# Optimization experiments

Measured on AMD Instinct MI355X. Metric: run time of the kernel, lower is better.

The kernel has to match this reference:

```python
import jax, jax.numpy as jnp
import numpy as np

N_NODES = 50000
N_EDGES = 800000
IN_CH, HID_CH, OUT_CH = 100, 128, 47
ORIG_SIZE = 25000


def sage_conv(x, edge_index, w_l, b_l, w_r):
    """PyG-style SAGEConv with mean aggregation.
    out = lin_l(mean_{j in N(i)} x_j) + lin_r(x_i)
    edge_index[0]=source, edge_index[1]=target.
    """
    src, dst = edge_index[0], edge_index[1]
    n = x.shape[0]
    # gather source features, scatter-sum into targets  [N, d]
    agg = jax.ops.segment_sum(x[src], dst, num_segments=n)
    deg = jax.ops.segment_sum(jnp.ones((src.shape[0],), x.dtype), dst, num_segments=n)
    mean = agg / jnp.maximum(deg, 1.0)[:, None]
    return mean @ w_l + b_l + x @ w_r


def setup_inputs() -> dict:
    key = jax.random.key(0)
    ks = jax.random.split(key, 8)
    x = jax.random.normal(ks[0], (N_NODES, IN_CH), dtype=jnp.float32)
    edge_index = jax.random.randint(ks[1], (2, N_EDGES), 0, N_NODES, dtype=jnp.int32)
    s1 = 1.0 / np.sqrt(IN_CH)
    s2 = 1.0 / np.sqrt(HID_CH)
    w1_l = jax.random.uniform(ks[2], (IN_CH, HID_CH), jnp.float32, -s1, s1)
    b1_l = jax.random.uniform(ks[3], (HID_CH,), jnp.float32, -s1, s1)
    w1_r = jax.random.uniform(ks[4], (IN_CH, HID_CH), jnp.float32, -s1, s1)
    w2_l = jax.random.uniform(ks[5], (HID_CH, OUT_CH), jnp.float32, -s2, s2)
    b2_l = jax.random.uniform(ks[6], (OUT_CH,), jnp.float32, -s2, s2)
    w2_r = jax.random.uniform(ks[7], (HID_CH, OUT_CH), jnp.float32, -s2, s2)
    return {"x": x, "edge_index": edge_index, "original_size": ORIG_SIZE,
            "w1_l": w1_l, "b1_l": b1_l, "w1_r": w1_r,
            "w2_l": w2_l, "b2_l": b2_l, "w2_r": w2_r}


def reference(x, edge_index, original_size, w1_l, b1_l, w1_r, w2_l, b2_l, w2_r):
    h = sage_conv(x, edge_index, w1_l, b1_l, w1_r)   # [N, hidden]
    h = sage_conv(h, edge_index, w2_l, b2_l, w2_r)   # [N, out]
    logp = jax.nn.log_softmax(h, axis=1)
    return logp[:original_size]
```

## Files before the change

kernel.cpp:

```cpp
#include <hip/hip_runtime.h>
#include <hip/hip_fp16.h>
#include <math.h>

constexpr int N    = 50000;
constexpr int E    = 800000;
constexpr int CIN  = 100;
constexpr int CH   = 128;
constexpr int COUT = 47;
constexpr int NOUT = 25000;
constexpr int CP   = 48;
constexpr int NB   = (N + 255) / 256;
constexpr int TN   = 128;
constexpr int NT   = (N + TN - 1) / TN;

constexpr int HS  = 136;
constexpr int W1K = 256;
constexpr int W2K = 128;
constexpr int A1S = 256;

constexpr int HB = (E + 255) / 256;
constexpr int CB = (N * 32) / 256;
constexpr int PB = 193;

typedef float f32x4 __attribute__((ext_vector_type(4)));
typedef short v8s  __attribute__((ext_vector_type(8)));

__device__ __forceinline__ void bsplit(float f, ushort& h, ushort& l) {
    uint u = __float_as_uint(f);
    h = (ushort)(u >> 16);
    float fh = __uint_as_float(u & 0xffff0000u);
    l = (ushort)(__float_as_uint(f - fh) >> 16);
}

__device__ __forceinline__ void unpack8(uint4 v, v8s& ah, v8s& al) {
    union { uint4 u; __half2 h[4]; } V; V.u = v;
    ushort hh[8], ll[8];
    #pragma unroll
    for (int p = 0; p < 4; ++p) {
        float2 f = __half22float2(V.h[p]);
        bsplit(f.x, hh[2 * p],     ll[2 * p]);
        bsplit(f.y, hh[2 * p + 1], ll[2 * p + 1]);
    }
    ah = v8s{(short)hh[0], (short)hh[1], (short)hh[2], (short)hh[3],
             (short)hh[4], (short)hh[5], (short)hh[6], (short)hh[7]};
    al = v8s{(short)ll[0], (short)ll[1], (short)ll[2], (short)ll[3],
             (short)ll[4], (short)ll[5], (short)ll[6], (short)ll[7]};
}

__global__ __launch_bounds__(256) void pre_kernel(
        const int* __restrict__ dst, int* __restrict__ cnt, int* __restrict__ rank,
        const float* __restrict__ x, __half* __restrict__ x16,
        __half* __restrict__ a1x,
        const float* __restrict__ w1l, const float* __restrict__ w1r,
        const float* __restrict__ w2l, const float* __restrict__ w2r,
        const float* __restrict__ b2l,
        ushort* __restrict__ w1T, ushort* __restrict__ w2T,
        float* __restrict__ b2cat) {
    int bid = blockIdx.x, t = threadIdx.x;
    if (bid < HB) {
        int i = bid * 256 + t;
        if (i < E) rank[i] = atomicAdd(&cnt[dst[i]], 1);
    } else if (bid < HB + CB) {
        int j = (bid - HB) * 256 + t;
        int row = j >> 5, s = j & 31;
        uint2 u = make_uint2(0u, 0u);
        if (s < 25) {
            float4 v = ((const float4*)x)[row * 25 + s];
            __half2 h0 = __floats2half2_rn(v.x, v.y);
            __half2 h1 = __floats2half2_rn(v.z, v.w);
            union { __half2 h[2]; uint2 u; } U;
            U.h[0] = h0; U.h[1] = h1;
            u = U.u;
            ((uint2*)x16)[row * 25 + s] = u;
        }
        ((uint2*)a1x)[(size_t)row * 64 + 32 + s] = u;
    } else {
        int i = (bid - HB - CB) * 256 + t;
        if (i < 128 * W1K) {
            int n = i >> 8, k = i & 255;
            float v = 0.0f;
            if (k < 100)                    v = w1l[(size_t)k * CH + n];
            else if (k >= 128 && k < 228)   v = w1r[(size_t)(k - 128) * CH + n];
            ushort h, l; bsplit(v, h, l);
            w1T[i] = h; w1T[128 * W1K + i] = l;
        } else if (i < 128 * W1K + 128 * W2K) {
            int j2 = i - 128 * W1K;
            int n = j2 >> 7, k = j2 & 127;
            float v = 0.0f;
            if (n < COUT)                      v = w2l[(size_t)k * COUT + n];
            else if (n >= 64 && n < 64 + COUT) v = w2r[(size_t)k * COUT + (n - 64)];
            ushort h, l; bsplit(v, h, l);
            w2T[j2] = h; w2T[128 * W2K + j2] = l;
        } else {
            int j2 = i - (128 * W1K + 128 * W2K);
            if (j2 < 128) b2cat[j2] = (j2 >= 64 && j2 < 64 + COUT) ? b2l[j2 - 64] : 0.0f;
        }
    }
}

__global__ __launch_bounds__(256) void scan_blocks(const int* __restrict__ cnt,
        int* __restrict__ row_ptr, int* __restrict__ blkSum) {
    __shared__ int s[256];
    int t = threadIdx.x;
    int i = blockIdx.x * 256 + t;
    int v = (i < N) ? cnt[i] : 0;
    s[t] = v;
    __syncthreads();
    for (int off = 1; off < 256; off <<= 1) {
        int a = s[t];
        int u = (t >= off) ? s[t - off] : 0;
        __syncthreads();
        s[t] = a + u;
        __syncthreads();
    }
    if (i < N) row_ptr[i] = s[t] - v;
    if (t == 255) blkSum[blockIdx.x] = s[255];
}

__global__ __launch_bounds__(256) void scan_apply(int* __restrict__ row_ptr,
        const int* __restrict__ blkSum) {
    __shared__ int s[256];
    int t = threadIdx.x, bid = blockIdx.x;
    int a = 0;
    for (int j = t; j < bid; j += 256) a += blkSum[j];
    s[t] = a;
    __syncthreads();
    for (int off = 128; off > 0; off >>= 1) {
        if (t < off) s[t] += s[t + off];
        __syncthreads();
    }
    int offset = s[0];
    int i = bid * 256 + t;
    if (i < N) {
        row_ptr[i] += offset;
        if (i == N - 1) row_ptr[N] = E;
    }
}

__global__ void fill_kernel(const int* __restrict__ src, const int* __restrict__ dst,
        const int* __restrict__ rank, const int* __restrict__ row_ptr,
        int* __restrict__ col) {
    int i = blockIdx.x * blockDim.x + threadIdx.x;
    if (i < E) col[row_ptr[dst[i]] + rank[i]] = src[i];
}

__global__ __launch_bounds__(256) void gather1_kernel(const __half* __restrict__ x16,
        const int* __restrict__ row_ptr, const int* __restrict__ col,
        __half* __restrict__ a1x) {
    int t = threadIdx.x;
    int n = blockIdx.x * 4 + (t >> 6);
    int l = t & 63, half = l >> 5, li = l & 31;
    int b = row_ptr[n], e = row_ptr[n + 1];
    float inv = 1.0f / (float)max(e - b, 1);
    const uint2* xb = (const uint2*)x16;
    bool act = li < 25;
    float4 s0 = make_float4(0.f, 0.f, 0.f, 0.f);
    float4 s1 = make_float4(0.f, 0.f, 0.f, 0.f);
    float4 s2 = make_float4(0.f, 0.f, 0.f, 0.f);
    float4 s3 = make_float4(0.f, 0.f, 0.f, 0.f);
    union { uint2 u; __half2 h[2]; } U0, U1, U2, U3;
    int j = b + half;
    for (; j + 6 < e; j += 8) {
        int c0 = col[j], c1 = col[j + 2], c2 = col[j + 4], c3 = col[j + 6];
        if (act) {
            U0.u = xb[(size_t)c0 * 25 + li];
            U1.u = xb[(size_t)c1 * 25 + li];
            U2.u = xb[(size_t)c2 * 25 + li];
            U3.u = xb[(size_t)c3 * 25 + li];
            float2 f0a = __half22float2(U0.h[0]), f0b = __half22float2(U0.h[1]);
            float2 f1a = __half22float2(U1.h[0]), f1b = __half22float2(U1.h[1]);
            float2 f2a = __half22float2(U2.h[0]), f2b = __half22float2(U2.h[1]);
            float2 f3a = __half22float2(U3.h[0]), f3b = __half22float2(U3.h[1]);
            s0.x += f0a.x; s0.y += f0a.y; s0.z += f0b.x; s0.w += f0b.y;
            s1.x += f1a.x; s1.y += f1a.y; s1.z += f1b.x; s1.w += f1b.y;
            s2.x += f2a.x; s2.y += f2a.y; s2.z += f2b.x; s2.w += f2b.y;
            s3.x += f3a.x; s3.y += f3a.y; s3.z += f3b.x; s3.w += f3b.y;
        }
    }
    for (; j < e; j += 2) {
        int c0 = col[j];
        if (act) {
            U0.u = xb[(size_t)c0 * 25 + li];
            float2 f0a = __half22float2(U0.h[0]), f0b = __half22float2(U0.h[1]);
            s0.x += f0a.x; s0.y += f0a.y; s0.z += f0b.x; s0.w += f0b.y;
        }
    }
    float4 s = make_float4(s0.x + s1.x + s2.x + s3.x,
                           s0.y + s1.y + s2.y + s3.y,
                           s0.z + s1.z + s2.z + s3.z,
                           s0.w + s1.w + s2.w + s3.w);
    s.x += __shfl_xor(s.x, 32, 64);
    s.y += __shfl_xor(s.y, 32, 64);
    s.z += __shfl_xor(s.z, 32, 64);
    s.w += __shfl_xor(s.w, 32, 64);
    if (half == 0) {
        __half2 p0 = __floats2half2_rn(s.x * inv, s.y * inv);
        __half2 p1 = __floats2half2_rn(s.z * inv, s.w * inv);
        union { __half2 h[2]; uint2 u; } P;
        P.h[0] = p0; P.h[1] = p1;
        ((uint2*)a1x)[(size_t)n * 64 + li] = P.u;
    }
}

__global__ __launch_bounds__(256) void fused_gemm(
        const __half* __restrict__ a1x,
        const ushort* __restrict__ w1T, const float* __restrict__ b1l,
        const ushort* __restrict__ w2T, const float* __restrict__ b2cat,
        __half* __restrict__ gsrc16, float* __restrict__ gself) {
    __shared__ __align__(16) uint lds_u[17408];
    ushort* Hh = (ushort*)lds_u;
    ushort* Hl = Hh + 128 * HS;

    int t = threadIdx.x;
    int lane = t & 63;
    int wv = __builtin_amdgcn_readfirstlane(t >> 6);
    int nh = wv & 1, chh = wv >> 1;
    int l15 = lane & 15, lg = lane >> 4;
    int base = blockIdx.x * TN;

    const ushort* w1Th = w1T;
    const ushort* w1Tl = w1T + 128 * W1K;
    const ushort* w2Th = w2T;
    const ushort* w2Tl = w2T + 128 * W2K;

    f32x4 acc[4][4];
    #pragma unroll
    for (int nt = 0; nt < 4; ++nt) {
        float bv = b1l[chh * 64 + nt * 16 + l15];
        #pragma unroll
        for (int mt = 0; mt < 4; ++mt)
            acc[mt][nt] = f32x4{bv, bv, bv, bv};
    }

    #pragma unroll 2
    for (int ks = 0; ks < 8; ++ks) {
        int k0 = ks * 32 + lg * 8;
        v8s ahf[4], alf[4];
        #pragma unroll
        for (int mt = 0; mt < 4; ++mt) {
            int row = base + nh * 64 + mt * 16 + l15;
            int rr = row < N ? row : N - 1;
            uint4 v = *(const uint4*)(a1x + (size_t)rr * A1S + k0);
            unpack8(v, ahf[mt], alf[mt]);
        }
        #pragma unroll
        for (int nt = 0; nt < 4; ++nt) {
            int n = chh * 64 + nt * 16 + l15;
            v8s bhf = *(const v8s*)(w1Th + (size_t)n * W1K + k0);
            v8s blf = *(const v8s*)(w1Tl + (size_t)n * W1K + k0);
            #pragma unroll
            for (int mt = 0; mt < 4; ++mt) {
                acc[mt][nt] = __builtin_amdgcn_mfma_f32_16x16x32_bf16(
                    ahf[mt], bhf, acc[mt][nt], 0, 0, 0);
                acc[mt][nt] = __builtin_amdgcn_mfma_f32_16x16x32_bf16(
                    alf[mt], bhf, acc[mt][nt], 0, 0, 0);
                acc[mt][nt] = __builtin_amdgcn_mfma_f32_16x16x32_bf16(
                    ahf[mt], blf, acc[mt][nt], 0, 0, 0);
            }
        }
    }

    #pragma unroll
    for (int mt = 0; mt < 4; ++mt) {
        #pragma unroll
        for (int nt = 0; nt < 4; ++nt) {
            int ch = chh * 64 + nt * 16 + l15;
            #pragma unroll
            for (int r = 0; r < 4; ++r) {
                int node = nh * 64 + mt * 16 + lg * 4 + r;
                ushort h, l; bsplit(acc[mt][nt][r], h, l);
                Hh[node * HS + ch] = h;
                Hl[node * HS + ch] = l;
            }
        }
    }
    __syncthreads();

    bool skip = (chh == 1) && (base >= NOUT);
    if (!skip) {
        #pragma unroll
        for (int nt = 0; nt < 4; ++nt) {
            float bv = b2cat[chh * 64 + nt * 16 + l15];
            #pragma unroll
            for (int mt = 0; mt < 4; ++mt)
                acc[mt][nt] = f32x4{bv, bv, bv, bv};
        }
        #pragma unroll
        for (int ks = 0; ks < 4; ++ks) {
            v8s ahf[4], alf[4];
            #pragma unroll
            for (int mt = 0; mt < 4; ++mt) {
                int node = nh * 64 + mt * 16 + l15;
                int ko = ks * 32 + lg * 8;
                ahf[mt] = *(const v8s*)(Hh + node * HS + ko);
                alf[mt] = *(const v8s*)(Hl + node * HS + ko);
            }
            int kg = ks * 32 + lg * 8;
            #pragma unroll
            for (int nt = 0; nt < 4; ++nt) {
                int n = chh * 64 + nt * 16 + l15;
                v8s bhf = *(const v8s*)(w2Th + (size_t)n * W2K + kg);
                v8s blf = *(const v8s*)(w2Tl + (size_t)n * W2K + kg);
                #pragma unroll
                for (int mt = 0; mt < 4; ++mt) {
                    acc[mt][nt] = __builtin_amdgcn_mfma_f32_16x16x32_bf16(
                        ahf[mt], bhf, acc[mt][nt], 0, 0, 0);
                    acc[mt][nt] = __builtin_amdgcn_mfma_f32_16x16x32_bf16(
                        alf[mt], bhf, acc[mt][nt], 0, 0, 0);
                    acc[mt][nt] = __builtin_amdgcn_mfma_f32_16x16x32_bf16(
                        ahf[mt], blf, acc[mt][nt], 0, 0, 0);
                }
            }
        }
        int lim = chh ? NOUT : N;
        #pragma unroll
        for (int nt = 0; nt < 3; ++nt) {
            int colc = nt * 16 + l15;
            #pragma unroll
            for (int mt = 0; mt < 4; ++mt) {
                #pragma unroll
                for (int r = 0; r < 4; ++r) {
                    int node = base + nh * 64 + mt * 16 + lg * 4 + r;
                    if (node < lim) {
                        if (chh) gself[(size_t)node * CP + colc] = acc[mt][nt][r];
                        else gsrc16[(size_t)node * CP + colc] =
                                 __float2half(acc[mt][nt][r]);
                    }
                }
            }
        }
    }
}

__global__ __launch_bounds__(256) void final_kernel(const __half* __restrict__ gsrc16,
        const float* __restrict__ gself, const int* __restrict__ row_ptr,
        const int* __restrict__ col, float* __restrict__ out) {
    int t = threadIdx.x;
    int n = blockIdx.x * 4 + (t >> 6);
    int c = t & 63;
    int b = row_ptr[n], e = row_ptr[n + 1];
    float inv = 1.0f / (float)max(e - b, 1);
    float a0 = 0.f, a1 = 0.f, a2 = 0.f, a3 = 0.f;
    if (c < CP) {
        int j = b;
        for (; j + 3 < e; j += 4) {
            a0 += __half2float(gsrc16[(size_t)col[j]     * CP + c]);
            a1 += __half2float(gsrc16[(size_t)col[j + 1] * CP + c]);
            a2 += __half2float(gsrc16[(size_t)col[j + 2] * CP + c]);
            a3 += __half2float(gsrc16[(size_t)col[j + 3] * CP + c]);
        }
        for (; j < e; ++j) a0 += __half2float(gsrc16[(size_t)col[j] * CP + c]);
    }
    float val = (c < COUT)
        ? (((a0 + a1) + (a2 + a3)) * inv + gself[(size_t)n * CP + c]) : -INFINITY;
    float m = val;
    #pragma unroll
    for (int off = 32; off > 0; off >>= 1) m = fmaxf(m, __shfl_xor(m, off, 64));
    float ex = (c < COUT) ? expf(val - m) : 0.f;
    float ssum = ex;
    #pragma unroll
    for (int off = 32; off > 0; off >>= 1) ssum += __shfl_xor(ssum, off, 64);
    if (c < COUT)
        __builtin_nontemporal_store(val - m - logf(ssum),
                                    out + (size_t)n * COUT + c);
}

extern "C" void kernel_launch(void* const* d_in, const int* in_sizes, int n_in,
                              void* d_out, int out_size, void* d_ws, size_t ws_size,
                              hipStream_t stream) {
    const float* x   = (const float*)d_in[0];
    const int*   ei  = (const int*)d_in[1];
    const int*   src = ei;
    const int*   dst = ei + E;
    const float* w1l = (const float*)d_in[3];
    const float* b1l = (const float*)d_in[4];
    const float* w1r = (const float*)d_in[5];
    const float* w2l = (const float*)d_in[6];
    const float* b2l = (const float*)d_in[7];
    const float* w2r = (const float*)d_in[8];
    float* out = (float*)d_out;

    int* cnt     = (int*)d_ws;
    int* row_ptr = cnt + N;
    int* rank    = row_ptr + N + 1;
    int* blkSum  = rank + E;
    int* col     = blkSum + NB;
    size_t intWords = (size_t)N + (N + 1) + E + NB + E;
    intWords = (intWords + 3) & ~(size_t)3;
    float* gself  = (float*)d_ws + intWords;
    float* b2cat  = gself + (size_t)NOUT * CP;
    __half* gsrc16 = (__half*)(b2cat + 128);
    __half* x16    = gsrc16 + (size_t)N * CP;
    __half* a1x    = x16 + (size_t)N * CIN;
    ushort* w1T   = (ushort*)(a1x + (size_t)N * A1S);
    ushort* w2T   = w1T + 2 * 128 * W1K;

    (void)hipMemsetAsync(cnt, 0, (size_t)N * sizeof(int), stream);
    pre_kernel  <<<HB + CB + PB, 256, 0, stream>>>(dst, cnt, rank, x, x16, a1x,
                                                   w1l, w1r, w2l, w2r, b2l,
                                                   w1T, w2T, b2cat);
    scan_blocks <<<NB, 256, 0, stream>>>(cnt, row_ptr, blkSum);
    scan_apply  <<<NB, 256, 0, stream>>>(row_ptr, blkSum);
    fill_kernel <<<(E + 255) / 256, 256, 0, stream>>>(src, dst, rank, row_ptr, col);
    gather1_kernel<<<N / 4, 256, 0, stream>>>(x16, row_ptr, col, a1x);
    fused_gemm  <<<NT, 256, 0, stream>>>(a1x, w1T, b1l, w2T, b2cat,
                                         gsrc16, gself);
    final_kernel<<<NOUT / 4, 256, 0, stream>>>(gsrc16, gself, row_ptr, col, out);
}
```

Measured before the change: 227.2 us.

## Build CSR with range-partitioned atomics and cursor-based fill, dropping rank array

The histogram and fill steps now assign each block a chunk of edges and one of eight destination ranges (by block index modulo 8), so each block's atomics land on a narrower slice of the count array, likely to improve cache locality. The per-edge rank array is removed: scan_apply writes a cursor copy of row_ptr, and fill uses atomicAdd on that cursor to place each source, which saves E ints of writes and reads. Each edge chunk is now read eight times, and the order of neighbours within a row is no longer deterministic, so float summation order can vary between runs.

After: 254.2 us. 1.12x slower.

```diff
diff --git a/kernel.cpp b/kernel.cpp
--- a/kernel.cpp
+++ b/kernel.cpp
@@ -18,7 +18,11 @@
 constexpr int W2K = 128;
 constexpr int A1S = 256;
 
-constexpr int HB = (E + 255) / 256;
+constexpr int RNG = N / 8;
+constexpr int ECH = 2048;
+constexpr int NCH = (E + ECH - 1) / ECH;
+constexpr int HB8 = 8 * NCH;
+
 constexpr int CB = (N * 32) / 256;
 constexpr int PB = 193;
 
@@ -48,7 +52,7 @@
 }
 
 __global__ __launch_bounds__(256) void pre_kernel(
-        const int* __restrict__ dst, int* __restrict__ cnt, int* __restrict__ rank,
+        const int* __restrict__ dst, int* __restrict__ cnt,
         const float* __restrict__ x, __half* __restrict__ x16,
         __half* __restrict__ a1x,
         const float* __restrict__ w1l, const float* __restrict__ w1r,
@@ -57,11 +61,21 @@
         ushort* __restrict__ w1T, ushort* __restrict__ w2T,
         float* __restrict__ b2cat) {
     int bid = blockIdx.x, t = threadIdx.x;
-    if (bid < HB) {
-        int i = bid * 256 + t;
-        if (i < E) rank[i] = atomicAdd(&cnt[dst[i]], 1);
-    } else if (bid < HB + CB) {
-        int j = (bid - HB) * 256 + t;
+    if (bid < HB8) {
+        int r = bid & 7, c = bid >> 3;
+        int e0 = c * ECH + t * 8;
+        if (e0 < E) {
+            int4 d0 = *(const int4*)(dst + e0);
+            int4 d1 = *(const int4*)(dst + e0 + 4);
+            int lo = r * RNG;
+            int dd[8] = {d0.x, d0.y, d0.z, d0.w, d1.x, d1.y, d1.z, d1.w};
+            #pragma unroll
+            for (int k = 0; k < 8; ++k)
+                if ((unsigned)(dd[k] - lo) < (unsigned)RNG)
+                    atomicAdd(&cnt[dd[k]], 1);
+        }
+    } else if (bid < HB8 + CB) {
+        int j = (bid - HB8) * 256 + t;
         int row = j >> 5, s = j & 31;
         uint2 u = make_uint2(0u, 0u);
         if (s < 25) {
@@ -75,7 +89,7 @@
         }
         ((uint2*)a1x)[(size_t)row * 64 + 32 + s] = u;
     } else {
-        int i = (bid - HB - CB) * 256 + t;
+        int i = (bid - HB8 - CB) * 256 + t;
         if (i < 128 * W1K) {
             int n = i >> 8, k = i & 255;
             float v = 0.0f;
@@ -118,7 +132,7 @@
 }
 
 __global__ __launch_bounds__(256) void scan_apply(int* __restrict__ row_ptr,
-        const int* __restrict__ blkSum) {
+        int* __restrict__ cursor, const int* __restrict__ blkSum) {
     __shared__ int s[256];
     int t = threadIdx.x, bid = blockIdx.x;
     int a = 0;
@@ -132,16 +146,32 @@
     int offset = s[0];
     int i = bid * 256 + t;
     if (i < N) {
-        row_ptr[i] += offset;
+        int v = row_ptr[i] + offset;
+        row_ptr[i] = v;
+        cursor[i]  = v;
         if (i == N - 1) row_ptr[N] = E;
     }
 }
 
 __global__ void fill_kernel(const int* __restrict__ src, const int* __restrict__ dst,
-        const int* __restrict__ rank, const int* __restrict__ row_ptr,
-        int* __restrict__ col) {
-    int i = blockIdx.x * blockDim.x + threadIdx.x;
-    if (i < E) col[row_ptr[dst[i]] + rank[i]] = src[i];
+        int* __restrict__ cursor, int* __restrict__ col) {
+    int r = blockIdx.x & 7, c = blockIdx.x >> 3;
+    int e0 = c * ECH + threadIdx.x * 8;
+    if (e0 >= E) return;
+    int4 d0 = *(const int4*)(dst + e0);
+    int4 d1 = *(const int4*)(dst + e0 + 4);
+    int4 s0 = *(const int4*)(src + e0);
+    int4 s1 = *(const int4*)(src + e0 + 4);
+    int lo = r * RNG;
+    int dd[8] = {d0.x, d0.y, d0.z, d0.w, d1.x, d1.y, d1.z, d1.w};
+    int ss[8] = {s0.x, s0.y, s0.z, s0.w, s1.x, s1.y, s1.z, s1.w};
+    #pragma unroll
+    for (int k = 0; k < 8; ++k) {
+        if ((unsigned)(dd[k] - lo) < (unsigned)RNG) {
+            int p = atomicAdd(&cursor[dd[k]], 1);
+            col[p] = ss[k];
+        }
+    }
 }
 
 __global__ __launch_bounds__(256) void gather1_kernel(const __half* __restrict__ x16,
@@ -382,10 +412,10 @@
 
     int* cnt     = (int*)d_ws;
     int* row_ptr = cnt + N;
-    int* rank    = row_ptr + N + 1;
-    int* blkSum  = rank + E;
+    int* cursor  = row_ptr + N + 1;
+    int* blkSum  = cursor + N;
     int* col     = blkSum + NB;
-    size_t intWords = (size_t)N + (N + 1) + E + NB + E;
+    size_t intWords = (size_t)N + (N + 1) + N + NB + E;
     intWords = (intWords + 3) & ~(size_t)3;
     float* gself  = (float*)d_ws + intWords;
     float* b2cat  = gself + (size_t)NOUT * CP;
@@ -396,12 +426,12 @@
     ushort* w2T   = w1T + 2 * 128 * W1K;
 
     (void)hipMemsetAsync(cnt, 0, (size_t)N * sizeof(int), stream);
-    pre_kernel  <<<HB + CB + PB, 256, 0, stream>>>(dst, cnt, rank, x, x16, a1x,
-                                                   w1l, w1r, w2l, w2r, b2l,
-                                                   w1T, w2T, b2cat);
+    pre_kernel  <<<HB8 + CB + PB, 256, 0, stream>>>(dst, cnt, x, x16, a1x,
+                                                    w1l, w1r, w2l, w2r, b2l,
+                                                    w1T, w2T, b2cat);
     scan_blocks <<<NB, 256, 0, stream>>>(cnt, row_ptr, blkSum);
-    scan_apply  <<<NB, 256, 0, stream>>>(row_ptr, blkSum);
-    fill_kernel <<<(E + 255) / 256, 256, 0, stream>>>(src, dst, rank, row_ptr, col);
+    scan_apply  <<<NB, 256, 0, stream>>>(row_ptr, cursor, blkSum);
+    fill_kernel <<<HB8, 256, 0, stream>>>(src, dst, cursor, col);
     gather1_kernel<<<N / 4, 256, 0, stream>>>(x16, row_ptr, col, a1x);
     fused_gemm  <<<NT, 256, 0, stream>>>(a1x, w1T, b1l, w2T, b2cat,
                                          gsrc16, gself);
```
